# Kernel optimization log

Measured on AMD Instinct MI355X. Metric: run time of the kernel, lower is better.

Reference implementation:

```python
import jax, jax.numpy as jnp
import numpy as np

B, T, E = 2, 2048, 2048
H, NOPE, ROPE, VD, KVR, DR = 16, 64, 32, 64, 256, 2
QKD = NOPE + ROPE  # 96
LOWR = KVR // 4    # hypernet low_rank=4 -> 64


def _rope_angles(position, dim):
    # freqs_cis angles: pos * 10000^(-2i/dim), matching torch rotary with theta=10000
    inv = jnp.exp(jnp.arange(0, dim, 2, dtype=jnp.float32) * (-jnp.log(jnp.float32(10000.0)) / dim))
    return position.astype(jnp.float32)[..., None] * inv  # (1, T, dim//2)


def _apply_rotary(x, ang):
    # x: (B,T,H,D); pairs are consecutive elements (view_as_complex semantics)
    x2 = x.reshape(x.shape[:-1] + (-1, 2))
    c = jnp.cos(ang)[:, :, None, :]
    s = jnp.sin(ang)[:, :, None, :]
    xr, xi = x2[..., 0], x2[..., 1]
    return jnp.stack([xr * c - xi * s, xr * s + xi * c], axis=-1).reshape(x.shape)


def _layernorm(x, g, b, eps=1e-5):
    m = jnp.mean(x, axis=-1, keepdims=True)
    v = jnp.var(x, axis=-1, keepdims=True)
    return (x - m) * jax.lax.rsqrt(v + eps) * g + b


def _sinusoid_pe(t, d):
    pos = jnp.arange(t, dtype=jnp.float32)[:, None]
    div = jnp.exp(jnp.arange(0, d, 2, dtype=jnp.float32) * (-jnp.log(jnp.float32(10000.0)) / d))
    pe = jnp.zeros((t, d), dtype=jnp.float32)
    pe = pe.at[:, 0::2].set(jnp.sin(pos * div)).at[:, 1::2].set(jnp.cos(pos * div))
    return pe


def setup_inputs() -> dict:
    key = jax.random.key(0)
    ks = jax.random.split(key, 16)
    sd = 0.02
    return {
        "query": jax.random.normal(ks[0], (B, T, E), jnp.float32),
        "key": jax.random.normal(ks[1], (B, T, E), jnp.float32),
        "value": jax.random.normal(ks[2], (B, T, E), jnp.float32),
        "position": jnp.arange(T, dtype=jnp.int32)[None, :],
        # weights stored transposed for right-multiply (x @ W)
        "wq": jax.random.normal(ks[3], (E, H * QKD), jnp.float32) * sd,
        "wkv_a": jax.random.normal(ks[4], (E, KVR + ROPE), jnp.float32) * sd,
        "kv_gamma": jnp.ones((KVR,), jnp.float32),
        "kv_beta": jnp.zeros((KVR,), jnp.float32),
        # torch layout (H*(NOPE+VD), KVR) kept for faithful view(H,-1,KVR) absorb
        "wkv_b": jax.random.normal(ks[5], (H * (NOPE + VD), KVR), jnp.float32) * sd,
        "wo": jax.random.normal(ks[6], (H * VD, E), jnp.float32) * sd,
        "fc_c_w": jax.random.normal(ks[7], (KVR, LOWR), jnp.float32) * sd,
        "fc_c_b": jnp.zeros((LOWR,), jnp.float32),
        "fc_p_w": jax.random.normal(ks[8], (KVR, LOWR), jnp.float32) * sd,
        "fc_p_b": jnp.zeros((LOWR,), jnp.float32),
    }


def reference(query, key, value, position, wq, wkv_a, kv_gamma, kv_beta, wkv_b, wo,
              fc_c_w, fc_c_b, fc_p_w, fc_p_b):
    bsz, seqlen, _ = query.shape
    # queries: low-rank-free path (q_lora_rank=0)
    q = (query @ wq).reshape(bsz, seqlen, H, QKD)
    q_nope, q_pe = q[..., :NOPE], q[..., NOPE:]
    ang = _rope_angles(position, ROPE)  # (1, T, ROPE//2)
    q_pe = _apply_rotary(q_pe, ang[:, -seqlen:])
    # key/value latent projection
    kv_all = key @ wkv_a  # (B, T, KVR+ROPE)
    kv, k_pe = kv_all[..., :KVR], kv_all[..., KVR:]
    k_pe = _apply_rotary(k_pe[:, :, None, :], ang)[:, :, 0, :]  # (B, T, ROPE)
    kv_norm = _layernorm(kv, kv_gamma, kv_beta)  # (B, T, KVR)
    # hypernetwork temporal downsampling weights (train path, T_input=kv_norm)
    t = -(-seqlen // DR)
    C = jnp.repeat(_sinusoid_pe(t, KVR), DR, axis=0)[:seqlen]  # (T, KVR)
    C2 = C @ fc_c_w + fc_c_b           # (T, LOWR)
    P2 = kv_norm @ fc_p_w + fc_p_b     # (B, T, LOWR)
    W = jax.nn.sigmoid(jnp.einsum('tc,bsc->bts', C2, P2))  # (B, T, T)
    idx = jnp.arange(seqlen)
    chunk = idx // DR
    # chunk mask: cumulative within-chunk causal accumulation
    zero_mask = ((chunk[:, None] == chunk[None, :]) & (idx[None, :] <= idx[:, None])).astype(query.dtype)
    kv_t = jnp.einsum('bts,bsc->btc', W * zero_mask, kv_norm)  # (B, T, KVR)
    # stride-aware causal mask: attend completed chunk-end slots + own in-progress slot
    allowed = (idx[None, :] == idx[:, None]) | ((idx[None, :] < idx[:, None]) & (((idx[None, :] + 1) % DR) == 0))
    attn_mask = jnp.where(allowed, jnp.float32(0.0), jnp.float32(-1e30))
    # absorbed MLA attention
    wb = wkv_b.reshape(H, NOPE + VD, KVR)
    q_abs = jnp.einsum('bshd,hdc->bshc', q_nope, wb[:, :NOPE])  # (B, S, H, KVR)
    scores = (jnp.einsum('bshc,btc->bsht', q_abs, kv_t)
              + jnp.einsum('bshr,btr->bsht', q_pe, k_pe)) * (QKD ** -0.5)
    scores = scores + attn_mask[None, :, None, :]
    attn = jax.nn.softmax(scores, axis=-1)
    x = jnp.einsum('bsht,btc->bshc', attn, kv_t)
    x = jnp.einsum('bshc,hdc->bshd', x, wb[:, NOPE:])  # (B, S, H, VD)
    return x.reshape(bsz, seqlen, H * VD) @ wo
```

## Files before the change

### kernel.cpp

```cpp
#include <hip/hip_runtime.h>
#include <stddef.h>

typedef unsigned short u16;
typedef unsigned short u16x8 __attribute__((ext_vector_type(8)));
typedef short s16x8 __attribute__((ext_vector_type(8)));
typedef float f32x4 __attribute__((ext_vector_type(4)));

#define B_ 2
#define T_ 2048
#define E_ 2048
#define H_ 16

__device__ inline float us2f(u16 u){
  unsigned int i = ((unsigned int)u) << 16;
  return __builtin_bit_cast(float, i);
}
__device__ inline u16 f2us(float f){
  unsigned int x = __builtin_bit_cast(unsigned int, f);
  unsigned int r = (x + 0x7fffu + ((x >> 16) & 1u)) >> 16;
  return (u16)r;
}
__device__ inline f32x4 mfma32(s16x8 a, s16x8 b, f32x4 c){
  return __builtin_amdgcn_mfma_f32_16x16x32_bf16(a, b, c, 0, 0, 0);
}
__device__ inline s16x8 ld8(const u16* p){
  return __builtin_bit_cast(s16x8, *(const u16x8*)p);
}
__device__ inline void gload_lds16(const u16* g, u16* l){
  __builtin_amdgcn_global_load_lds(
      (const __attribute__((address_space(1))) unsigned int*)(g),
      (__attribute__((address_space(3))) unsigned int*)(l), 16, 0, 0);
}

__global__ void transpose_f32_bf16(const float* __restrict__ in, u16* __restrict__ out, int R, int C)
{
  __shared__ float tile[32][33];
  int c0 = blockIdx.x * 32, r0 = blockIdx.y * 32;
  int tx = threadIdx.x, ty = threadIdx.y;
  for (int i = ty; i < 32; i += 8){
    int r = r0 + i, c = c0 + tx;
    tile[i][tx] = (r < R && c < C) ? in[(size_t)r * C + c] : 0.f;
  }
  __syncthreads();
  for (int i = ty; i < 32; i += 8){
    int c = c0 + i, r = r0 + tx;
    if (c < C && r < R) out[(size_t)c * R + r] = f2us(tile[tx][i]);
  }
}

__global__ __launch_bounds__(256) void cvt_f32_bf16(const float* __restrict__ in,
    u16* __restrict__ out, int n)
{
  int i = (blockIdx.x * 256 + threadIdx.x) * 4;
  if (i + 3 < n){
    f32x4 v = *(const f32x4*)(in + i);
    out[i]   = f2us(v[0]); out[i+1] = f2us(v[1]);
    out[i+2] = f2us(v[2]); out[i+3] = f2us(v[3]);
  }
}

template<int A_F32, int OUT_F32>
__global__ __launch_bounds__(256) void gemm_bt(const void* __restrict__ Ap,
    const u16* __restrict__ Bt, void* __restrict__ Cp, int M, int N, int K)
{
  __shared__ __align__(16) u16 As[64][40];
  __shared__ __align__(16) u16 Bs[64][40];
  const int tid  = threadIdx.x;
  const int lane = tid & 63;
  const int wid  = tid >> 6;
  const int quad = lane >> 4;
  const int col  = lane & 15;
  const int bm = blockIdx.y * 64;
  const int bn = blockIdx.x * 64;
  const int lr = tid >> 2;
  const int lc = (tid & 3) * 8;
  const int waveM = wid >> 1, waveN = wid & 1;

  f32x4 acc[2][2];
  for (int i = 0; i < 2; ++i)
    for (int j = 0; j < 2; ++j)
      acc[i][j] = (f32x4){0.f, 0.f, 0.f, 0.f};

  const u16x8 zero8 = {0,0,0,0,0,0,0,0};
  const bool bok = (bn + lr) < N;
  const u16*   arow16 = (const u16*)Ap   + (size_t)(bm + lr) * K + lc;
  const float* arow32 = (const float*)Ap + (size_t)(bm + lr) * K + lc;
  const u16* brow = Bt + (size_t)(bn + lr) * K + lc;

  for (int kk = 0; kk < K; kk += 32) {
    u16x8 av;
    if (A_F32) {
      f32x4 a0 = *(const f32x4*)(arow32 + kk);
      f32x4 a1 = *(const f32x4*)(arow32 + kk + 4);
      av[0]=f2us(a0[0]); av[1]=f2us(a0[1]); av[2]=f2us(a0[2]); av[3]=f2us(a0[3]);
      av[4]=f2us(a1[0]); av[5]=f2us(a1[1]); av[6]=f2us(a1[2]); av[7]=f2us(a1[3]);
    } else {
      av = *(const u16x8*)(arow16 + kk);
    }
    u16x8 bv = bok ? *(const u16x8*)(brow + kk) : zero8;
    __syncthreads();
    *(u16x8*)&As[lr][lc] = av;
    *(u16x8*)&Bs[lr][lc] = bv;
    __syncthreads();
    s16x8 af0 = ld8(&As[waveM*32 + col][quad*8]);
    s16x8 af1 = ld8(&As[waveM*32 + 16 + col][quad*8]);
    s16x8 bf0 = ld8(&Bs[waveN*32 + col][quad*8]);
    s16x8 bf1 = ld8(&Bs[waveN*32 + 16 + col][quad*8]);
    acc[0][0] = mfma32(af0, bf0, acc[0][0]);
    acc[0][1] = mfma32(af0, bf1, acc[0][1]);
    acc[1][0] = mfma32(af1, bf0, acc[1][0]);
    acc[1][1] = mfma32(af1, bf1, acc[1][1]);
  }
  for (int am = 0; am < 2; ++am)
    for (int bnn = 0; bnn < 2; ++bnn)
      for (int i = 0; i < 4; ++i) {
        int r = bm + waveM*32 + am*16 + quad*4 + i;
        int c = bn + waveN*32 + bnn*16 + col;
        if (c < N){
          if (OUT_F32) ((float*)Cp)[(size_t)r * N + c] = acc[am][bnn][i];
          else         ((u16*)Cp)[(size_t)r * N + c]   = f2us(acc[am][bnn][i]);
        }
      }
}

template<int OUT_F32>
__global__ __launch_bounds__(256) void gemm128(const u16* __restrict__ A,
    const u16* __restrict__ Bt, void* __restrict__ Cp, int M, int N, int K)
{
  __shared__ __align__(16) u16 As[128 * 32];
  __shared__ __align__(16) u16 Bs[128 * 32];
  const int tid  = threadIdx.x;
  const int lane = tid & 63;
  const int wid  = tid >> 6;
  const int quad = lane >> 4;
  const int col  = lane & 15;
  const int bm = blockIdx.y * 128;
  const int bn = blockIdx.x * 128;
  const int waveM = wid >> 1, waveN = wid & 1;

  const int srow = wid * 16 + (lane >> 2);
  const int scol = (lane & 3) * 8;
  const u16* ga = A  + (size_t)(bm + srow) * K + scol;
  const u16* gb = Bt + (size_t)(bn + srow) * K + scol;
  const size_t rowskip = (size_t)64 * K;
  u16* lAs0 = &As[wid * 512];
  u16* lAs1 = &As[wid * 512 + 2048];
  u16* lBs0 = &Bs[wid * 512];
  u16* lBs1 = &Bs[wid * 512 + 2048];

  f32x4 acc[4][4] = {};

  for (int kk = 0; kk < K; kk += 32) {
    __syncthreads();
    gload_lds16(ga + kk,           lAs0);
    gload_lds16(ga + rowskip + kk, lAs1);
    gload_lds16(gb + kk,           lBs0);
    gload_lds16(gb + rowskip + kk, lBs1);
    __syncthreads();
    s16x8 af[4], bf[4];
#pragma unroll
    for (int i = 0; i < 4; ++i) af[i] = ld8(&As[(waveM*64 + i*16 + col) * 32 + quad*8]);
#pragma unroll
    for (int i = 0; i < 4; ++i) bf[i] = ld8(&Bs[(waveN*64 + i*16 + col) * 32 + quad*8]);
#pragma unroll
    for (int i = 0; i < 4; ++i)
#pragma unroll
      for (int j = 0; j < 4; ++j)
        acc[i][j] = mfma32(af[i], bf[j], acc[i][j]);
  }
#pragma unroll
  for (int i = 0; i < 4; ++i)
#pragma unroll
    for (int j = 0; j < 4; ++j)
#pragma unroll
      for (int r = 0; r < 4; ++r) {
        int row = bm + waveM*64 + i*16 + quad*4 + r;
        int c   = bn + waveN*64 + j*16 + col;
        if (OUT_F32) ((float*)Cp)[(size_t)row * N + c] = acc[i][j][r];
        else         ((u16*)Cp)[(size_t)row * N + c]   = f2us(acc[i][j][r]);
      }
}

__global__ __launch_bounds__(256) void qsplit(const u16* __restrict__ qtmp,
    const int* __restrict__ pos, u16* __restrict__ qh)
{
  int idx = blockIdx.x * 256 + threadIdx.x;
  if (idx >= B_*T_*H_*12) return;
  int c    = idx % 12;
  int rest = idx / 12;
  int h    = rest & 15;
  int row  = rest >> 4;
  int t    = row & (T_ - 1);
  int b    = row >> 11;
  const u16* src = qtmp + (size_t)row * 1536 + h * 96;
  u16* dst = qh + ((size_t)(b * 16 + h) * T_ + t) * 96;
  u16x8 v = *(const u16x8*)(src + c * 8);
  if (c >= 8) {
    int i0 = (c - 8) * 4;
    float pp = (float)pos[t];
#pragma unroll
    for (int k = 0; k < 4; ++k){
      int i = i0 + k;
      float ang = pp * __expf((float)(2*i) * -0.28782313657f);
      float cs = __cosf(ang), sn = __sinf(ang);
      float xr = us2f(v[2*k]), xi = us2f(v[2*k+1]);
      v[2*k]   = f2us(xr * cs - xi * sn);
      v[2*k+1] = f2us(xr * sn + xi * cs);
    }
  }
  *(u16x8*)(dst + c * 8) = v;
}

__global__ __launch_bounds__(256) void ln_p2_rope(
    const u16* __restrict__ kvall, const float* __restrict__ gamma,
    const float* __restrict__ beta, const float* __restrict__ fcpw,
    const float* __restrict__ fcpb, const int* __restrict__ pos,
    u16* __restrict__ kvn, float* __restrict__ P2, u16* __restrict__ kpe)
{
  const int row = blockIdx.x;
  if (row >= B_ * T_) return;
  const int tid = threadIdx.x;
  const int lane = tid & 63, wid = tid >> 6;
  __shared__ float kvs[256];
  __shared__ float part[256];
  __shared__ float redS[4], redS2[4];
  const u16* src = kvall + (size_t)row * 288;
  float v = us2f(src[tid]);
  float s1 = v, s2 = v * v;
  for (int off = 1; off < 64; off <<= 1){
    s1 += __shfl_xor(s1, off);
    s2 += __shfl_xor(s2, off);
  }
  if (lane == 0){ redS[wid] = s1; redS2[wid] = s2; }
  __syncthreads();
  float S  = redS[0] + redS[1] + redS[2] + redS[3];
  float Q  = redS2[0] + redS2[1] + redS2[2] + redS2[3];
  float mean = S * (1.f / 256.f);
  float var  = Q * (1.f / 256.f) - mean * mean;
  float rstd = rsqrtf(var + 1e-5f);
  float xn = (v - mean) * rstd * gamma[tid] + beta[tid];
  kvs[tid] = xn;
  kvn[(size_t)row * 256 + tid] = f2us(xn);
  __syncthreads();
  {
    int oc = tid & 63, pp = tid >> 6;
    float acc = 0.f;
#pragma unroll 8
    for (int c = pp * 64; c < pp * 64 + 64; ++c)
      acc += kvs[c] * fcpw[c * 64 + oc];
    part[tid] = acc;
  }
  __syncthreads();
  if (tid < 64) {
    P2[(size_t)row * 64 + tid] = fcpb[tid] + part[tid] + part[64 + tid]
                               + part[128 + tid] + part[192 + tid];
  } else if (tid < 80) {
    int i = tid - 64;
    int t = row & (T_ - 1);
    float ang = (float)pos[t] * __expf((float)(2*i) * -0.28782313657f);
    float c = __cosf(ang), s = __sinf(ang);
    float xr = us2f(src[256 + 2*i]);
    float xi = us2f(src[257 + 2*i]);
    kpe[(size_t)row * 32 + 2*i]     = f2us(xr * c - xi * s);
    kpe[(size_t)row * 32 + 2*i + 1] = f2us(xr * s + xi * c);
  }
}

__global__ __launch_bounds__(64) void c2_kernel(const float* __restrict__ fccw,
    const float* __restrict__ fccb, float* __restrict__ C2)
{
  const int t = blockIdx.x, tid = threadIdx.x;
  __shared__ float pe[256];
  float p = (float)(t >> 1);
  for (int i = tid; i < 128; i += 64){
    float div = expf((float)(2*i) * -0.03597789207f);
    float a = p * div;
    pe[2*i]   = sinf(a);
    pe[2*i+1] = cosf(a);
  }
  __syncthreads();
  float acc = fccb[tid];
  for (int c = 0; c < 256; ++c) acc += pe[c] * fccw[c * 64 + tid];
  C2[t * 64 + tid] = acc;
}

__global__ __launch_bounds__(64) void kvt_kernel(const float* __restrict__ C2,
    const float* __restrict__ P2, const u16* __restrict__ kvn, u16* __restrict__ kvt)
{
  const int row = blockIdx.x;
  if (row >= B_ * T_) return;
  const int lane = threadIdx.x;
  const int t = row & (T_ - 1);
  float c2v = C2[t * 64 + lane];
  float da = c2v * P2[(size_t)row * 64 + lane];
  for (int off = 1; off < 64; off <<= 1) da += __shfl_xor(da, off);
  float wtt = 1.f / (1.f + __expf(-da));
  const bool odd = (t & 1);
  float wts = 0.f;
  if (odd){
    float db = c2v * P2[(size_t)(row - 1) * 64 + lane];
    for (int off = 1; off < 64; off <<= 1) db += __shfl_xor(db, off);
    wts = 1.f / (1.f + __expf(-db));
  }
  for (int c = lane; c < 256; c += 64){
    float val = wtt * us2f(kvn[(size_t)row * 256 + c]);
    if (odd) val += wts * us2f(kvn[(size_t)(row - 1) * 256 + c]);
    kvt[(size_t)row * 256 + c] = f2us(val);
  }
}

__global__ __launch_bounds__(256) void vt_kernel(const u16* __restrict__ kvb, u16* __restrict__ Vt)
{
  const int bid = blockIdx.x;
  const int jt = bid & 15;
  const int h  = (bid >> 4) & 15;
  const int b  = bid >> 8;
  const int tid = threadIdx.x;
  __shared__ __align__(16) u16 tile[64][72];
  const int jl = tid >> 2;
  const int dseg = (tid & 3) * 16;
  const int j0 = jt * 64;
  {
    int s_ = 2 * (j0 + jl) + 1;
    const u16* src = kvb + ((size_t)(b * T_ + s_)) * 2048 + h * 128 + 64 + dseg;
    *(u16x8*)&tile[jl][dseg]     = *(const u16x8*)(src);
    *(u16x8*)&tile[jl][dseg + 8] = *(const u16x8*)(src + 8);
  }
  __syncthreads();
  const int dl = tid >> 2;
  const int jseg = (tid & 3) * 16;
  u16* dst = Vt + ((size_t)(b * 16 + h) * 64 + dl) * 1024 + j0 + jseg;
  u16x8 o;
  for (int r = 0; r < 8; ++r) o[r] = tile[jseg + r][dl];
  *(u16x8*)dst = o;
  for (int r = 0; r < 8; ++r) o[r] = tile[jseg + 8 + r][dl];
  *(u16x8*)(dst + 8) = o;
}

__global__ __launch_bounds__(256) void kc_gather(const u16* __restrict__ kvb,
    const u16* __restrict__ kpe, u16* __restrict__ Kc)
{
  int idx = blockIdx.x * 256 + threadIdx.x;
  int c  = idx % 12;
  int j  = (idx / 12) & 1023;
  int bh = idx / (12 * 1024);
  if (bh >= B_ * H_) return;
  int b = bh >> 4, h = bh & 15;
  int t = 2 * j + 1;
  u16x8 v;
  if (c < 8) v = *(const u16x8*)(kvb + ((size_t)(b * T_ + t)) * 2048 + h * 128 + c * 8);
  else       v = *(const u16x8*)(kpe + ((size_t)(b * T_ + t)) * 32 + (c - 8) * 8);
  *(u16x8*)(Kc + ((size_t)bh * 1024 + j) * 96 + c * 8) = v;
}

__global__ __launch_bounds__(256) void attn_kernel(
    const u16* __restrict__ qh, const u16* __restrict__ kvb,
    const u16* __restrict__ kpe, const u16* __restrict__ Kc,
    const u16* __restrict__ Vt, u16* __restrict__ xout)
{
  __shared__ __align__(16) u16 Ks[128 * 96];
  __shared__ __align__(16) u16 Vs[64][136];
  __shared__ __align__(16) u16 pbufA[4][16 * 136];
  const int tid  = threadIdx.x;
  const int wid  = tid >> 6;
  const int lane = tid & 63;
  const int quad = lane >> 4;
  const int col  = lane & 15;
  const int pair = blockIdx.x & 15;
  const int h    = (blockIdx.x >> 4) & 15;
  const int b    = blockIdx.x >> 8;
  const int bh   = b * H_ + h;
  u16* pbuf = pbufA[wid];
  const float scale = 0.10206207262f;
  const u16* KcH = Kc + (size_t)bh * 1024 * 96;
  const u16* VtH = Vt + (size_t)bh * 64 * 1024;

  for (int ph = 0; ph < 2; ++ph) {
    const int qt = ph ? (31 - pair) : pair;
    const int t0 = qt * 64 + wid * 16;

    s16x8 aq0, aq1, aq2;
    {
      const u16* qrow = qh + ((size_t)bh * T_ + t0 + col) * 96;
      aq0 = ld8(qrow + quad * 8);
      aq1 = ld8(qrow + 32 + quad * 8);
      aq2 = ld8(qrow + 64 + quad * 8);
    }
    float sself;
    {
      const int t = t0 + col;
      const u16* qrow = qh + ((size_t)bh * T_ + t) * 96;
      const u16* ka = kvb + ((size_t)(b * T_ + t)) * 2048 + h * 128;
      const u16* kp = kpe + ((size_t)(b * T_ + t)) * 32;
      float a = 0.f;
      for (int d = 0; d < 64; ++d) a += us2f(qrow[d]) * us2f(ka[d]);
      for (int d = 0; d < 32; ++d) a += us2f(qrow[64 + d]) * us2f(kp[d]);
      sself = a * scale;
    }
    float es[4], lacc[4];
    f32x4 O[4];
#pragma unroll
    for (int i = 0; i < 4; ++i){
      es[i] = __expf(__shfl(sself, quad * 4 + i));
      lacc[i] = 0.f;
    }
#pragma unroll
    for (int nt = 0; nt < 4; ++nt)
#pragma unroll
      for (int i = 0; i < 4; ++i){
        int t = t0 + quad * 4 + i;
        O[nt][i] = es[i] * us2f(kvb[((size_t)(b * T_ + t)) * 2048 + h * 128 + 64 + nt * 16 + col]);
      }

    const int nb = (qt * 32 + 31 + 127) >> 7;
    for (int blk = 0; blk < nb; ++blk) {
      const int jb = blk * 128;
      __syncthreads();
      {
        const u16* gk = KcH + (size_t)jb * 96 + (size_t)(wid * 6) * 512 + lane * 8;
        u16* lk = &Ks[(wid * 6) * 512];
#pragma unroll
        for (int k = 0; k < 6; ++k)
          gload_lds16(gk + k * 512, lk + k * 512);
        int d = tid >> 2, c4 = tid & 3;
        const u16* gv = VtH + (size_t)d * 1024 + jb + c4 * 32;
        u16* lv = &Vs[d][c4 * 32];
#pragma unroll
        for (int k = 0; k < 4; ++k)
          *(u16x8*)(lv + k * 8) = *(const u16x8*)(gv + k * 8);
      }
      __syncthreads();
#pragma unroll
      for (int cc = 0; cc < 4; ++cc){
        const u16* k0 = &Ks[(cc * 32 + col) * 96];
        const u16* k1 = &Ks[(cc * 32 + 16 + col) * 96];
        f32x4 s0 = {0,0,0,0}, s1 = {0,0,0,0};
        s0 = mfma32(aq0, ld8(k0 + quad * 8), s0);
        s0 = mfma32(aq1, ld8(k0 + 32 + quad * 8), s0);
        s0 = mfma32(aq2, ld8(k0 + 64 + quad * 8), s0);
        s1 = mfma32(aq0, ld8(k1 + quad * 8), s1);
        s1 = mfma32(aq1, ld8(k1 + 32 + quad * 8), s1);
        s1 = mfma32(aq2, ld8(k1 + 64 + quad * 8), s1);
        int key0 = jb + cc * 32 + col;
#pragma unroll
        for (int i = 0; i < 4; ++i){
          int lim = (t0 + quad * 4 + i) >> 1;
          float p0 = (key0 < lim)      ? __expf(s0[i] * scale) : 0.f;
          float p1 = (key0 + 16 < lim) ? __expf(s1[i] * scale) : 0.f;
          lacc[i] += p0 + p1;
          pbuf[(quad * 4 + i) * 136 + cc * 32 + col]      = f2us(p0);
          pbuf[(quad * 4 + i) * 136 + cc * 32 + 16 + col] = f2us(p1);
        }
      }
      asm volatile("s_waitcnt lgkmcnt(0)" ::: "memory");
#pragma unroll
      for (int cc = 0; cc < 4; ++cc){
        s16x8 pf = ld8(&pbuf[col * 136 + cc * 32 + quad * 8]);
#pragma unroll
        for (int nt = 0; nt < 4; ++nt)
          O[nt] = mfma32(pf, ld8(&Vs[nt * 16 + col][cc * 32 + quad * 8]), O[nt]);
      }
    }
#pragma unroll
    for (int i = 0; i < 4; ++i){
      float l = lacc[i];
      l += __shfl_xor(l, 1);
      l += __shfl_xor(l, 2);
      l += __shfl_xor(l, 4);
      l += __shfl_xor(l, 8);
      lacc[i] = es[i] + l;
    }
#pragma unroll
    for (int nt = 0; nt < 4; ++nt)
#pragma unroll
      for (int i = 0; i < 4; ++i){
        int t = t0 + quad * 4 + i;
        xout[((size_t)(b * T_ + t)) * 1024 + h * 64 + nt * 16 + col] = f2us(O[nt][i] / lacc[i]);
      }
    __syncthreads();
  }
}

extern "C" void kernel_launch(void* const* d_in, const int* in_sizes, int n_in,
                              void* d_out, int out_size, void* d_ws, size_t ws_size,
                              hipStream_t stream)
{
  (void)in_sizes; (void)n_in; (void)out_size; (void)ws_size;
  const float* query = (const float*)d_in[0];
  const float* key_  = (const float*)d_in[1];
  const int*   pos   = (const int*)d_in[3];
  const float* wq    = (const float*)d_in[4];
  const float* wkva  = (const float*)d_in[5];
  const float* gamma = (const float*)d_in[6];
  const float* beta  = (const float*)d_in[7];
  const float* wkvb  = (const float*)d_in[8];
  const float* wo    = (const float*)d_in[9];
  const float* fccw  = (const float*)d_in[10];
  const float* fccb  = (const float*)d_in[11];
  const float* fcpw  = (const float*)d_in[12];
  const float* fcpb  = (const float*)d_in[13];

  char* p = (char*)d_ws;
  auto alloc = [&](size_t bytes) -> void* {
    void* r = (void*)p;
    p += (bytes + 255) & ~(size_t)255;
    return r;
  };
  u16* wqT    = (u16*)alloc(1536ull * 2048 * 2);
  u16* wkvaT  = (u16*)alloc(288ull  * 2048 * 2);
  u16* woT    = (u16*)alloc(2048ull * 1024 * 2);
  u16* wkvbB  = (u16*)alloc(2048ull * 256 * 2);
  u16* queryB = (u16*)alloc(4096ull * 2048 * 2);
  u16* keyB   = (u16*)alloc(4096ull * 2048 * 2);
  u16* qtmp   = (u16*)alloc(4096ull * 1536 * 2);
  u16* qh     = (u16*)alloc(65536ull * 96 * 2);
  u16* kvall  = (u16*)alloc(4096ull * 288 * 2);
  u16* kvn    = (u16*)alloc(4096ull * 256 * 2);
  u16* kpe    = (u16*)alloc(4096ull * 32 * 2);
  float* P2   = (float*)alloc(4096ull * 64 * 4);
  float* C2   = (float*)alloc(2048ull * 64 * 4);
  u16* kvt    = (u16*)alloc(4096ull * 256 * 2);
  u16* kvb    = (u16*)alloc(4096ull * 2048 * 2);
  u16* Kc     = (u16*)alloc(32ull * 1024 * 96 * 2);
  u16* Vt     = (u16*)alloc(2048ull * 1024 * 2);
  u16* x      = (u16*)alloc(4096ull * 1024 * 2);

  dim3 tb(32, 8);
  transpose_f32_bf16<<<dim3(48, 64), tb, 0, stream>>>(wq,   wqT,   2048, 1536);
  transpose_f32_bf16<<<dim3(9,  64), tb, 0, stream>>>(wkva, wkvaT, 2048, 288);
  transpose_f32_bf16<<<dim3(64, 32), tb, 0, stream>>>(wo,   woT,   1024, 2048);
  cvt_f32_bf16<<<512,  256, 0, stream>>>(wkvb,  wkvbB,  2048 * 256);
  cvt_f32_bf16<<<8192, 256, 0, stream>>>(query, queryB, 4096 * 2048);
  cvt_f32_bf16<<<8192, 256, 0, stream>>>(key_,  keyB,   4096 * 2048);

  gemm128<0><<<dim3(12, 32), 256, 0, stream>>>(queryB, wqT, qtmp, 4096, 1536, 2048);
  gemm_bt<0,0><<<dim3(5, 64), 256, 0, stream>>>(keyB, wkvaT, kvall, 4096, 288, 2048);

  qsplit<<<3072, 256, 0, stream>>>(qtmp, pos, qh);
  ln_p2_rope<<<4096, 256, 0, stream>>>(kvall, gamma, beta, fcpw, fcpb, pos, kvn, P2, kpe);
  c2_kernel<<<2048, 64, 0, stream>>>(fccw, fccb, C2);
  kvt_kernel<<<4096, 64, 0, stream>>>(C2, P2, kvn, kvt);

  gemm128<0><<<dim3(16, 32), 256, 0, stream>>>(kvt, wkvbB, kvb, 4096, 2048, 256);
  vt_kernel<<<512, 256, 0, stream>>>(kvb, Vt);
  kc_gather<<<1536, 256, 0, stream>>>(kvb, kpe, Kc);
  attn_kernel<<<512, 256, 0, stream>>>(qh, kvb, kpe, Kc, Vt, x);

  gemm128<1><<<dim3(16, 32), 256, 0, stream>>>(x, woT, d_out, 4096, 2048, 1024);
}
```

Baseline: 392.8 us.

## Merge prep kernels, split-K the Q projection, and parallelize c2 computation

Fuses the three weight transposes and the wkv_b conversion into one launch, merges the query/key conversions into one, and merges the V-transpose and K-gather kernels into one, cutting launch count. The Q projection GEMM becomes a split-K kernel with two partial bf16 outputs that qsplit sums, doubling the grid to fill more CUs on the mi355x. c2_kernel moves to 256 threads with a 4-way reduction and fast intrinsics. Summing partials rounded to bf16 adds rounding error and extra memory traffic.

```diff
diff --git a/kernel.cpp b/kernel.cpp
--- a/kernel.cpp
+++ b/kernel.cpp
@@ -32,27 +32,47 @@
       (__attribute__((address_space(3))) unsigned int*)(l), 16, 0, 0);
 }
 
-__global__ void transpose_f32_bf16(const float* __restrict__ in, u16* __restrict__ out, int R, int C)
+__global__ __launch_bounds__(256) void prep_weights(
+    const float* __restrict__ wq, const float* __restrict__ wkva,
+    const float* __restrict__ wo, const float* __restrict__ wkvb,
+    u16* __restrict__ wqT, u16* __restrict__ wkvaT, u16* __restrict__ woT,
+    u16* __restrict__ wkvbB)
 {
   __shared__ float tile[32][33];
-  int c0 = blockIdx.x * 32, r0 = blockIdx.y * 32;
-  int tx = threadIdx.x, ty = threadIdx.y;
-  for (int i = ty; i < 32; i += 8){
-    int r = r0 + i, c = c0 + tx;
-    tile[i][tx] = (r < R && c < C) ? in[(size_t)r * C + c] : 0.f;
-  }
-  __syncthreads();
-  for (int i = ty; i < 32; i += 8){
-    int c = c0 + i, r = r0 + tx;
-    if (c < C && r < R) out[(size_t)c * R + r] = f2us(tile[tx][i]);
-  }
-}
-
-__global__ __launch_bounds__(256) void cvt_f32_bf16(const float* __restrict__ in,
-    u16* __restrict__ out, int n)
-{
-  int i = (blockIdx.x * 256 + threadIdx.x) * 4;
-  if (i + 3 < n){
+  const int bid = blockIdx.x;
+  const int tid = threadIdx.x;
+  if (bid < 5696) {
+    const float* in; u16* out; int R, C, bx, by;
+    if (bid < 3072)      { in = wq;   out = wqT;   R = 2048; C = 1536; bx = bid % 48;          by = bid / 48; }
+    else if (bid < 3648) { in = wkva; out = wkvaT; R = 2048; C = 288;  bx = (bid-3072) % 9;    by = (bid-3072) / 9; }
+    else                 { in = wo;   out = woT;   R = 1024; C = 2048; bx = (bid-3648) % 64;   by = (bid-3648) / 64; }
+    int tx = tid & 31, ty = tid >> 5;
+    int c0 = bx * 32, r0 = by * 32;
+    for (int i = ty; i < 32; i += 8){
+      int r = r0 + i, c = c0 + tx;
+      tile[i][tx] = (r < R && c < C) ? in[(size_t)r * C + c] : 0.f;
+    }
+    __syncthreads();
+    for (int i = ty; i < 32; i += 8){
+      int c = c0 + i, r = r0 + tx;
+      if (c < C && r < R) out[(size_t)c * R + r] = f2us(tile[tx][i]);
+    }
+  } else {
+    int i = (bid - 5696) * 1024 + tid * 4;
+    f32x4 v = *(const f32x4*)(wkvb + i);
+    wkvbB[i]   = f2us(v[0]); wkvbB[i+1] = f2us(v[1]);
+    wkvbB[i+2] = f2us(v[2]); wkvbB[i+3] = f2us(v[3]);
+  }
+}
+
+__global__ __launch_bounds__(256) void cvt2_f32_bf16(const float* __restrict__ a,
+    const float* __restrict__ b, u16* __restrict__ oa, u16* __restrict__ ob, int n_each)
+{
+  int idx = (blockIdx.x * 256 + threadIdx.x) * 4;
+  const float* in; u16* out; int i;
+  if (idx < n_each){ in = a; out = oa; i = idx; }
+  else             { in = b; out = ob; i = idx - n_each; }
+  if (i + 3 < n_each){
     f32x4 v = *(const f32x4*)(in + i);
     out[i]   = f2us(v[0]); out[i+1] = f2us(v[1]);
     out[i+2] = f2us(v[2]); out[i+3] = f2us(v[3]);
@@ -181,8 +201,67 @@
       }
 }
 
-__global__ __launch_bounds__(256) void qsplit(const u16* __restrict__ qtmp,
-    const int* __restrict__ pos, u16* __restrict__ qh)
+__global__ __launch_bounds__(256) void gemm128_sk(const u16* __restrict__ A,
+    const u16* __restrict__ Bt, u16* __restrict__ Cp0, u16* __restrict__ Cp1,
+    int M, int N, int K, int Klen)
+{
+  __shared__ __align__(16) u16 As[128 * 32];
+  __shared__ __align__(16) u16 Bs[128 * 32];
+  const int tid  = threadIdx.x;
+  const int lane = tid & 63;
+  const int wid  = tid >> 6;
+  const int quad = lane >> 4;
+  const int col  = lane & 15;
+  const int bm = blockIdx.y * 128;
+  const int bn = blockIdx.x * 128;
+  const int kh = blockIdx.z;
+  const int waveM = wid >> 1, waveN = wid & 1;
+
+  const int srow = wid * 16 + (lane >> 2);
+  const int scol = (lane & 3) * 8;
+  const u16* ga = A  + (size_t)(bm + srow) * K + kh * Klen + scol;
+  const u16* gb = Bt + (size_t)(bn + srow) * K + kh * Klen + scol;
+  const size_t rowskip = (size_t)64 * K;
+  u16* lAs0 = &As[wid * 512];
+  u16* lAs1 = &As[wid * 512 + 2048];
+  u16* lBs0 = &Bs[wid * 512];
+  u16* lBs1 = &Bs[wid * 512 + 2048];
+  u16* Cp = kh ? Cp1 : Cp0;
+
+  f32x4 acc[4][4] = {};
+
+  for (int kk = 0; kk < Klen; kk += 32) {
+    __syncthreads();
+    gload_lds16(ga + kk,           lAs0);
+    gload_lds16(ga + rowskip + kk, lAs1);
+    gload_lds16(gb + kk,           lBs0);
+    gload_lds16(gb + rowskip + kk, lBs1);
+    __syncthreads();
+    s16x8 af[4], bf[4];
+#pragma unroll
+    for (int i = 0; i < 4; ++i) af[i] = ld8(&As[(waveM*64 + i*16 + col) * 32 + quad*8]);
+#pragma unroll
+    for (int i = 0; i < 4; ++i) bf[i] = ld8(&Bs[(waveN*64 + i*16 + col) * 32 + quad*8]);
+#pragma unroll
+    for (int i = 0; i < 4; ++i)
+#pragma unroll
+      for (int j = 0; j < 4; ++j)
+        acc[i][j] = mfma32(af[i], bf[j], acc[i][j]);
+  }
+#pragma unroll
+  for (int i = 0; i < 4; ++i)
+#pragma unroll
+    for (int j = 0; j < 4; ++j)
+#pragma unroll
+      for (int r = 0; r < 4; ++r) {
+        int row = bm + waveM*64 + i*16 + quad*4 + r;
+        int c   = bn + waveN*64 + j*16 + col;
+        Cp[(size_t)row * N + c] = f2us(acc[i][j][r]);
+      }
+}
+
+__global__ __launch_bounds__(256) void qsplit(const u16* __restrict__ qp0,
+    const u16* __restrict__ qp1, const int* __restrict__ pos, u16* __restrict__ qh)
 {
   int idx = blockIdx.x * 256 + threadIdx.x;
   if (idx >= B_*T_*H_*12) return;
@@ -192,10 +271,14 @@
   int row  = rest >> 4;
   int t    = row & (T_ - 1);
   int b    = row >> 11;
-  const u16* src = qtmp + (size_t)row * 1536 + h * 96;
-  u16* dst = qh + ((size_t)(b * 16 + h) * T_ + t) * 96;
-  u16x8 v = *(const u16x8*)(src + c * 8);
-  if (c >= 8) {
+  size_t off = (size_t)row * 1536 + h * 96 + c * 8;
+  u16x8 v0 = *(const u16x8*)(qp0 + off);
+  u16x8 v1 = *(const u16x8*)(qp1 + off);
+  u16x8 v;
+  if (c < 8) {
+#pragma unroll
+    for (int k = 0; k < 8; ++k) v[k] = f2us(us2f(v0[k]) + us2f(v1[k]));
+  } else {
     int i0 = (c - 8) * 4;
     float pp = (float)pos[t];
 #pragma unroll
@@ -203,11 +286,13 @@
       int i = i0 + k;
       float ang = pp * __expf((float)(2*i) * -0.28782313657f);
       float cs = __cosf(ang), sn = __sinf(ang);
-      float xr = us2f(v[2*k]), xi = us2f(v[2*k+1]);
+      float xr = us2f(v0[2*k])   + us2f(v1[2*k]);
+      float xi = us2f(v0[2*k+1]) + us2f(v1[2*k+1]);
       v[2*k]   = f2us(xr * cs - xi * sn);
       v[2*k+1] = f2us(xr * sn + xi * cs);
     }
   }
+  u16* dst = qh + ((size_t)(b * 16 + h) * T_ + t) * 96;
   *(u16x8*)(dst + c * 8) = v;
 }
 
@@ -266,22 +351,32 @@
   }
 }
 
-__global__ __launch_bounds__(64) void c2_kernel(const float* __restrict__ fccw,
+__global__ __launch_bounds__(256) void c2_kernel(const float* __restrict__ fccw,
     const float* __restrict__ fccb, float* __restrict__ C2)
 {
   const int t = blockIdx.x, tid = threadIdx.x;
   __shared__ float pe[256];
+  __shared__ float part[256];
   float p = (float)(t >> 1);
-  for (int i = tid; i < 128; i += 64){
-    float div = expf((float)(2*i) * -0.03597789207f);
+  if (tid < 128){
+    float div = __expf((float)(2*tid) * -0.03597789207f);
     float a = p * div;
-    pe[2*i]   = sinf(a);
-    pe[2*i+1] = cosf(a);
+    pe[2*tid]   = __sinf(a);
+    pe[2*tid+1] = __cosf(a);
   }
   __syncthreads();
-  float acc = fccb[tid];
-  for (int c = 0; c < 256; ++c) acc += pe[c] * fccw[c * 64 + tid];
-  C2[t * 64 + tid] = acc;
+  {
+    int oc = tid & 63, pp = tid >> 6;
+    float acc = 0.f;
+#pragma unroll 8
+    for (int c = pp * 64; c < pp * 64 + 64; ++c)
+      acc += pe[c] * fccw[c * 64 + oc];
+    part[tid] = acc;
+  }
+  __syncthreads();
+  if (tid < 64)
+    C2[t * 64 + tid] = fccb[tid] + part[tid] + part[64 + tid]
+                     + part[128 + tid] + part[192 + tid];
 }
 
 __global__ __launch_bounds__(64) void kvt_kernel(const float* __restrict__ C2,
@@ -309,48 +404,47 @@
   }
 }
 
-__global__ __launch_bounds__(256) void vt_kernel(const u16* __restrict__ kvb, u16* __restrict__ Vt)
-{
-  const int bid = blockIdx.x;
-  const int jt = bid & 15;
-  const int h  = (bid >> 4) & 15;
-  const int b  = bid >> 8;
+__global__ __launch_bounds__(256) void vtkc_kernel(const u16* __restrict__ kvb,
+    const u16* __restrict__ kpe, u16* __restrict__ Vt, u16* __restrict__ Kc)
+{
+  __shared__ __align__(16) u16 tile[64][72];
   const int tid = threadIdx.x;
-  __shared__ __align__(16) u16 tile[64][72];
-  const int jl = tid >> 2;
-  const int dseg = (tid & 3) * 16;
-  const int j0 = jt * 64;
-  {
-    int s_ = 2 * (j0 + jl) + 1;
-    const u16* src = kvb + ((size_t)(b * T_ + s_)) * 2048 + h * 128 + 64 + dseg;
-    *(u16x8*)&tile[jl][dseg]     = *(const u16x8*)(src);
-    *(u16x8*)&tile[jl][dseg + 8] = *(const u16x8*)(src + 8);
-  }
-  __syncthreads();
-  const int dl = tid >> 2;
-  const int jseg = (tid & 3) * 16;
-  u16* dst = Vt + ((size_t)(b * 16 + h) * 64 + dl) * 1024 + j0 + jseg;
-  u16x8 o;
-  for (int r = 0; r < 8; ++r) o[r] = tile[jseg + r][dl];
-  *(u16x8*)dst = o;
-  for (int r = 0; r < 8; ++r) o[r] = tile[jseg + 8 + r][dl];
-  *(u16x8*)(dst + 8) = o;
-}
-
-__global__ __launch_bounds__(256) void kc_gather(const u16* __restrict__ kvb,
-    const u16* __restrict__ kpe, u16* __restrict__ Kc)
-{
-  int idx = blockIdx.x * 256 + threadIdx.x;
-  int c  = idx % 12;
-  int j  = (idx / 12) & 1023;
-  int bh = idx / (12 * 1024);
-  if (bh >= B_ * H_) return;
-  int b = bh >> 4, h = bh & 15;
-  int t = 2 * j + 1;
-  u16x8 v;
-  if (c < 8) v = *(const u16x8*)(kvb + ((size_t)(b * T_ + t)) * 2048 + h * 128 + c * 8);
-  else       v = *(const u16x8*)(kpe + ((size_t)(b * T_ + t)) * 32 + (c - 8) * 8);
-  *(u16x8*)(Kc + ((size_t)bh * 1024 + j) * 96 + c * 8) = v;
+  if (blockIdx.x < 512) {
+    const int bid = blockIdx.x;
+    const int jt = bid & 15;
+    const int h  = (bid >> 4) & 15;
+    const int b  = bid >> 8;
+    const int jl = tid >> 2;
+    const int dseg = (tid & 3) * 16;
+    const int j0 = jt * 64;
+    {
+      int s_ = 2 * (j0 + jl) + 1;
+      const u16* src = kvb + ((size_t)(b * T_ + s_)) * 2048 + h * 128 + 64 + dseg;
+      *(u16x8*)&tile[jl][dseg]     = *(const u16x8*)(src);
+      *(u16x8*)&tile[jl][dseg + 8] = *(const u16x8*)(src + 8);
+    }
+    __syncthreads();
+    const int dl = tid >> 2;
+    const int jseg = (tid & 3) * 16;
+    u16* dst = Vt + ((size_t)(b * 16 + h) * 64 + dl) * 1024 + j0 + jseg;
+    u16x8 o;
+    for (int r = 0; r < 8; ++r) o[r] = tile[jseg + r][dl];
+    *(u16x8*)dst = o;
+    for (int r = 0; r < 8; ++r) o[r] = tile[jseg + 8 + r][dl];
+    *(u16x8*)(dst + 8) = o;
+  } else {
+    int idx = (blockIdx.x - 512) * 256 + tid;
+    int c  = idx % 12;
+    int j  = (idx / 12) & 1023;
+    int bh = idx / (12 * 1024);
+    if (bh >= B_ * H_) return;
+    int b = bh >> 4, h = bh & 15;
+    int t = 2 * j + 1;
+    u16x8 v;
+    if (c < 8) v = *(const u16x8*)(kvb + ((size_t)(b * T_ + t)) * 2048 + h * 128 + c * 8);
+    else       v = *(const u16x8*)(kpe + ((size_t)(b * T_ + t)) * 32 + (c - 8) * 8);
+    *(u16x8*)(Kc + ((size_t)bh * 1024 + j) * 96 + c * 8) = v;
+  }
 }
 
 __global__ __launch_bounds__(256) void attn_kernel(
@@ -512,7 +606,8 @@
   u16* wkvbB  = (u16*)alloc(2048ull * 256 * 2);
   u16* queryB = (u16*)alloc(4096ull * 2048 * 2);
   u16* keyB   = (u16*)alloc(4096ull * 2048 * 2);
-  u16* qtmp   = (u16*)alloc(4096ull * 1536 * 2);
+  u16* qp0    = (u16*)alloc(4096ull * 1536 * 2);
+  u16* qp1    = (u16*)alloc(4096ull * 1536 * 2);
   u16* qh     = (u16*)alloc(65536ull * 96 * 2);
   u16* kvall  = (u16*)alloc(4096ull * 288 * 2);
   u16* kvn    = (u16*)alloc(4096ull * 256 * 2);
@@ -525,25 +620,19 @@
   u16* Vt     = (u16*)alloc(2048ull * 1024 * 2);
   u16* x      = (u16*)alloc(4096ull * 1024 * 2);
 
-  dim3 tb(32, 8);
-  transpose_f32_bf16<<<dim3(48, 64), tb, 0, stream>>>(wq,   wqT,   2048, 1536);
-  transpose_f32_bf16<<<dim3(9,  64), tb, 0, stream>>>(wkva, wkvaT, 2048, 288);
-  transpose_f32_bf16<<<dim3(64, 32), tb, 0, stream>>>(wo,   woT,   1024, 2048);
-  cvt_f32_bf16<<<512,  256, 0, stream>>>(wkvb,  wkvbB,  2048 * 256);
-  cvt_f32_bf16<<<8192, 256, 0, stream>>>(query, queryB, 4096 * 2048);
-  cvt_f32_bf16<<<8192, 256, 0, stream>>>(key_,  keyB,   4096 * 2048);
-
-  gemm128<0><<<dim3(12, 32), 256, 0, stream>>>(queryB, wqT, qtmp, 4096, 1536, 2048);
+  prep_weights<<<6208, 256, 0, stream>>>(wq, wkva, wo, wkvb, wqT, wkvaT, woT, wkvbB);
+  cvt2_f32_bf16<<<16384, 256, 0, stream>>>(query, key_, queryB, keyB, 4096 * 2048);
+
+  gemm128_sk<<<dim3(12, 32, 2), 256, 0, stream>>>(queryB, wqT, qp0, qp1, 4096, 1536, 2048, 1024);
   gemm_bt<0,0><<<dim3(5, 64), 256, 0, stream>>>(keyB, wkvaT, kvall, 4096, 288, 2048);
 
-  qsplit<<<3072, 256, 0, stream>>>(qtmp, pos, qh);
+  qsplit<<<3072, 256, 0, stream>>>(qp0, qp1, pos, qh);
   ln_p2_rope<<<4096, 256, 0, stream>>>(kvall, gamma, beta, fcpw, fcpb, pos, kvn, P2, kpe);
-  c2_kernel<<<2048, 64, 0, stream>>>(fccw, fccb, C2);
+  c2_kernel<<<2048, 256, 0, stream>>>(fccw, fccb, C2);
   kvt_kernel<<<4096, 64, 0, stream>>>(C2, P2, kvn, kvt);
 
   gemm128<0><<<dim3(16, 32), 256, 0, stream>>>(kvt, wkvbB, kvb, 4096, 2048, 256);
-  vt_kernel<<<512, 256, 0, stream>>>(kvb, Vt);
-  kc_gather<<<1536, 256, 0, stream>>>(kvb, kpe, Kc);
+  vtkc_kernel<<<2048, 256, 0, stream>>>(kvb, kpe, Vt, Kc);
   attn_kernel<<<512, 256, 0, stream>>>(qh, kvb, kpe, Kc, Vt, x);
 
   gemm128<1><<<dim3(16, 32), 256, 0, stream>>>(x, woT, d_out, 4096, 2048, 1024);
```

Result: faster. 362.7 us (-7.7%).
